# Kernel optimization log

Measured on AMD Instinct MI355X. Metric: run time of the kernel, lower is better.

The kernel has to match this reference:

```python
import jax, jax.numpy as jnp
import numpy as np

N_NODES = 100000
N_EDGES = 100000
D = 256
N_SIDE = 2  # rel_list = [side_a, side_b, rel_c, rel_d]
N_REL = 2


def setup_inputs() -> dict:
    key = jax.random.key(0)
    ks = jax.random.split(key, 7)
    h = jax.random.normal(ks[0], (N_NODES, D), dtype=jnp.float32)
    src_idx = jax.random.randint(ks[1], (N_SIDE + N_REL, N_EDGES), 0, N_NODES)
    dst_idx = jax.random.randint(ks[2], (N_SIDE + N_REL, N_EDGES), 0, N_NODES)
    # shared bilinear matrix R (nn.Linear(D, D, bias=False): y = x @ R_W.T)
    R_W = jax.random.normal(ks[3], (D, D), dtype=jnp.float32) * (1.0 / np.sqrt(D))
    # per-'side*' diagonal parameters (xavier over [D,1] then squeeze)
    d_side = jax.random.normal(ks[4], (N_SIDE, D), dtype=jnp.float32)
    # per-regular-relation Linear weights (with bias)
    W_rel = jax.random.normal(ks[5], (N_REL, D, D), dtype=jnp.float32) * (1.0 / np.sqrt(D))
    b_rel = jax.random.normal(ks[6], (N_REL, D), dtype=jnp.float32) * 0.01
    return {"h": h, "src_idx": src_idx, "dst_idx": dst_idx,
            "R_W": R_W, "d_side": d_side, "W_rel": W_rel, "b_rel": b_rel}


def reference(h, src_idx, dst_idx, R_W, d_side, W_rel, b_rel):
    # --- 'side*' edge types: score = (((h_u * d) @ R_W.T) * d) . h_v ---
    hu_s = h[src_idx[:N_SIDE]]            # [S, E, D] gather
    hv_s = h[dst_idx[:N_SIDE]]            # [S, E, D]
    lft = hu_s * d_side[:, None, :]       # [S, E, D]
    lft = jnp.einsum('sed,fd->sef', lft, R_W)  # Linear, no bias
    lft = lft * d_side[:, None, :]
    score_side = jnp.einsum('sed,sed->se', lft, hv_s)  # [S, E]

    # --- regular edge types: score = (h_u @ W.T + b) . h_v ---
    hu_r = h[src_idx[N_SIDE:]]            # [R, E, D]
    hv_r = h[dst_idx[N_SIDE:]]            # [R, E, D]
    lft_r = jnp.einsum('red,rfd->ref', hu_r, W_rel) + b_rel[:, None, :]
    score_rel = jnp.einsum('red,red->re', lft_r, hv_r)  # [R, E]

    return jnp.concatenate([score_side, score_rel], axis=0)  # [S+R, E]
```

## Files before the change

kernel.cpp:

```cpp
#include <hip/hip_runtime.h>
#include <stdint.h>

#define NNODES 100000
#define NEDGES 100000
#define DIM    256
#define NCH    4
#define ET     64
#define NT     1563
#define NBX    64
#define RSF    264
#define CONVB  2048
#define ZEROB  391

typedef _Float16 f16x8 __attribute__((ext_vector_type(8)));
typedef _Float16 f16x4 __attribute__((ext_vector_type(4)));
typedef float f32x4  __attribute__((ext_vector_type(4)));

__global__ void prep_fused(const float* __restrict__ RW,
                           const float* __restrict__ dside,
                           const float* __restrict__ Wrel,
                           const float* __restrict__ h,
                           _Float16* __restrict__ Bh, _Float16* __restrict__ Bl,
                           _Float16* __restrict__ H16,
                           float* __restrict__ out) {
    if (blockIdx.x < 128) {
        int t = blockIdx.x * blockDim.x + threadIdx.x;
        int lane = t & 63;
        int ft   = (t >> 6) & 15;
        int kc   = (t >> 10) & 7;
        int c    = t >> 13;
        int quad = lane >> 4, col = lane & 15;
        int f     = ft * 16 + col;
        int kbase = kc * 32 + quad * 8;

        f16x8 vh, vl;
#pragma unroll
        for (int j = 0; j < 8; ++j) {
            int k = kbase + j;
            float val;
            if (c < 2) {
                val = dside[c * DIM + f] * RW[f * DIM + k] * dside[c * DIM + k];
            } else {
                val = Wrel[(size_t)(c - 2) * DIM * DIM + f * DIM + k];
            }
            _Float16 hi = (_Float16)val;
            vh[j] = hi;
            vl[j] = (_Float16)(val - (float)hi);
        }
        ((f16x8*)Bh)[t] = vh;
        ((f16x8*)Bl)[t] = vl;
    } else if (blockIdx.x < 128 + ZEROB) {
        int i4 = (blockIdx.x - 128) * 256 + (int)threadIdx.x;
        if (i4 < NCH * NEDGES / 4)
            ((f32x4*)out)[i4] = (f32x4){0.f, 0.f, 0.f, 0.f};
    } else {
        const int total4 = NNODES * DIM / 4;
        const int stride = CONVB * 256;
        int i = (blockIdx.x - 128 - ZEROB) * 256 + (int)threadIdx.x;
        const f32x4* s4 = (const f32x4*)h;
        f16x4* d4 = (f16x4*)H16;
        for (; i + stride < total4; i += 2 * stride) {
            f32x4 a = s4[i];
            f32x4 b = s4[i + stride];
            f16x4 oa, ob;
#pragma unroll
            for (int j = 0; j < 4; ++j) { oa[j] = (_Float16)a[j]; ob[j] = (_Float16)b[j]; }
            d4[i] = oa; d4[i + stride] = ob;
        }
        if (i < total4) {
            f32x4 a = s4[i];
            f16x4 o;
#pragma unroll
            for (int j = 0; j < 4; ++j) o[j] = (_Float16)a[j];
            d4[i] = o;
        }
    }
}

__device__ __forceinline__ float dpp_reduce16(float s) {
    union { float f; int i; } u, v;
    u.f = s; v.i = __builtin_amdgcn_update_dpp(0, u.i, 0xB1,  0xF, 0xF, true); s += v.f;
    u.f = s; v.i = __builtin_amdgcn_update_dpp(0, u.i, 0x4E,  0xF, 0xF, true); s += v.f;
    u.f = s; v.i = __builtin_amdgcn_update_dpp(0, u.i, 0x141, 0xF, 0xF, true); s += v.f;
    u.f = s; v.i = __builtin_amdgcn_update_dpp(0, u.i, 0x140, 0xF, 0xF, true); s += v.f;
    return s;
}

__global__ __launch_bounds__(512, 1)
void edge_kernel(const _Float16* __restrict__ H16,
                 const int* __restrict__ src_idx,
                 const int* __restrict__ dst_idx,
                 const float* __restrict__ brel,
                 const _Float16* __restrict__ Bh_sw,
                 const _Float16* __restrict__ Bl_sw,
                 float* __restrict__ out) {
    const int c    = blockIdx.y;
    const int tid  = threadIdx.x;
    const int w    = tid >> 6;
    const int lane = tid & 63;
    const int quad = lane >> 4, col = lane & 15;

    __shared__ __align__(16) _Float16 s_a0[ET * RSF];
    __shared__ __align__(16) _Float16 s_v0[ET * RSF];
    __shared__ __align__(16) _Float16 s_a1[ET * RSF];
    __shared__ __align__(16) _Float16 s_v1[ET * RSF];

    f16x8 Bh_r[8][2], Bl_r[8][2];
    {
        const f16x8* bh = (const f16x8*)Bh_sw;
        const f16x8* bl = (const f16x8*)Bl_sw;
#pragma unroll
        for (int kc = 0; kc < 8; ++kc)
#pragma unroll
            for (int ftl = 0; ftl < 2; ++ftl) {
                int o = ((c * 8 + kc) * 16 + (w * 2 + ftl)) * 64 + lane;
                Bh_r[kc][ftl] = bh[o];
                Bl_r[kc][ftl] = bl[o];
            }
    }
#pragma unroll
    for (int kc = 0; kc < 8; ++kc)
#pragma unroll
        for (int ftl = 0; ftl < 2; ++ftl)
            asm volatile("" : "+v"(Bh_r[kc][ftl]), "+v"(Bl_r[kc][ftl]));

    float bias[2];
#pragma unroll
    for (int ftl = 0; ftl < 2; ++ftl) {
        int f = (w * 2 + ftl) * 16 + col;
        bias[ftl] = (c >= 2) ? brel[(size_t)(c - 2) * DIM + f] : 0.f;
    }

    const int  j8   = lane & 7;
    const bool isV  = (lane & 8) != 0;
    const int* ibase = (isV ? dst_idx : src_idx) + (size_t)c * NEDGES;

    auto loadpack = [&](int t) -> int {
        int e = t * ET + w * 8 + j8;
        if (e >= NEDGES) e = NEDGES - 1;
        return ibase[e];
    };

    const int t0 = blockIdx.x;
    f16x4 pA[8], pV[8];
    {
        int ip = loadpack(t0);
#pragma unroll
        for (int i = 0; i < 8; ++i) {
            int ia = __builtin_amdgcn_readlane(ip, i);
            int iv = __builtin_amdgcn_readlane(ip, 8 + i);
            pA[i] = *(const f16x4*)(H16 + (size_t)ia * DIM + lane * 4);
            pV[i] = *(const f16x4*)(H16 + (size_t)iv * DIM + lane * 4);
        }
    }
    int ipk0 = 0, ipk1 = 0;
    if (t0 + NBX < NT) ipk1 = loadpack(t0 + NBX);

    auto body = [&](int t, _Float16* sa, _Float16* sv, int& ipkUse, int& ipkLoad) {
#pragma unroll
        for (int i = 0; i < 8; ++i) {
            int lr = w * 8 + i;
            *(f16x4*)&sa[lr * RSF + lane * 4] = pA[i];
            *(f16x4*)&sv[lr * RSF + lane * 4] = pV[i];
        }

        if (t + 2 * NBX < NT) ipkLoad = loadpack(t + 2 * NBX);
        if (t + NBX < NT) {
#pragma unroll
            for (int i = 0; i < 8; ++i) {
                int ia = __builtin_amdgcn_readlane(ipkUse, i);
                int iv = __builtin_amdgcn_readlane(ipkUse, 8 + i);
                pA[i] = *(const f16x4*)(H16 + (size_t)ia * DIM + lane * 4);
                pV[i] = *(const f16x4*)(H16 + (size_t)iv * DIM + lane * 4);
            }
        }

        __syncthreads();

        f32x4 acc[4][2];
#pragma unroll
        for (int mt = 0; mt < 4; ++mt)
#pragma unroll
            for (int ftl = 0; ftl < 2; ++ftl) acc[mt][ftl] = (f32x4){0.f, 0.f, 0.f, 0.f};

#pragma unroll
        for (int kc = 0; kc < 8; ++kc) {
            f16x8 A[4];
#pragma unroll
            for (int mt = 0; mt < 4; ++mt)
                A[mt] = *(const f16x8*)&sa[(mt * 16 + col) * RSF + kc * 32 + quad * 8];
#pragma unroll
            for (int ftl = 0; ftl < 2; ++ftl) {
#pragma unroll
                for (int mt = 0; mt < 4; ++mt)
                    acc[mt][ftl] = __builtin_amdgcn_mfma_f32_16x16x32_f16(A[mt], Bh_r[kc][ftl], acc[mt][ftl], 0, 0, 0);
#pragma unroll
                for (int mt = 0; mt < 4; ++mt)
                    acc[mt][ftl] = __builtin_amdgcn_mfma_f32_16x16x32_f16(A[mt], Bl_r[kc][ftl], acc[mt][ftl], 0, 0, 0);
            }
        }

#pragma unroll
        for (int mt = 0; mt < 4; ++mt) {
            float ps[4];
#pragma unroll
            for (int r = 0; r < 4; ++r) {
                int el = mt * 16 + quad * 4 + r;
                float s = 0.f;
#pragma unroll
                for (int ftl = 0; ftl < 2; ++ftl) {
                    int f = (w * 2 + ftl) * 16 + col;
                    float v = (float)sv[el * RSF + f];
                    s += (acc[mt][ftl][r] + bias[ftl]) * v;
                }
                ps[r] = dpp_reduce16(s);
            }
            if (col == 0) {
#pragma unroll
                for (int r = 0; r < 4; ++r) {
                    int e = t * ET + mt * 16 + quad * 4 + r;
                    if (e < NEDGES)
                        atomicAdd(&out[(size_t)c * NEDGES + e], ps[r]);
                }
            }
        }
    };

    int t = t0;
    while (true) {
        body(t, s_a0, s_v0, ipk1, ipk0);
        t += NBX; if (t >= NT) break;
        body(t, s_a1, s_v1, ipk0, ipk1);
        t += NBX; if (t >= NT) break;
    }
}

extern "C" void kernel_launch(void* const* d_in, const int* in_sizes, int n_in,
                              void* d_out, int out_size, void* d_ws, size_t ws_size,
                              hipStream_t stream) {
    const float* hmat  = (const float*)d_in[0];
    const int*   src   = (const int*)d_in[1];
    const int*   dst   = (const int*)d_in[2];
    const float* RW    = (const float*)d_in[3];
    const float* dside = (const float*)d_in[4];
    const float* Wrel  = (const float*)d_in[5];
    const float* brel  = (const float*)d_in[6];
    float* out = (float*)d_out;

    const size_t nB = (size_t)NCH * DIM * DIM;
    _Float16* Bh  = (_Float16*)d_ws;
    _Float16* Bl  = Bh + nB;
    _Float16* H16 = Bl + nB;

    prep_fused<<<dim3(128 + ZEROB + CONVB), dim3(256), 0, stream>>>(
        RW, dside, Wrel, hmat, Bh, Bl, H16, out);

    dim3 grid(NBX, NCH);
    edge_kernel<<<grid, dim3(512), 0, stream>>>(H16, src, dst, brel, Bh, Bl, out);
}
```

Measured before the change: 290.3 us.

## Replace per-edge global atomics with LDS cross-wave reduction and direct stores

Each wave now writes its per-edge partial scores into a double-buffered shared array. The previous tile's eight partials are summed by 64 threads after the next tile's barrier, and the result is written with a plain store. This removes the global atomicAdd traffic and the separate zero-fill of the output in the prep kernel. In exchange it adds a small LDS buffer and a final barrier-and-reduce step after the loop.

```diff
diff --git a/kernel.cpp b/kernel.cpp
--- a/kernel.cpp
+++ b/kernel.cpp
@@ -10,7 +10,6 @@
 #define NBX    64
 #define RSF    264
 #define CONVB  2048
-#define ZEROB  391
 
 typedef _Float16 f16x8 __attribute__((ext_vector_type(8)));
 typedef _Float16 f16x4 __attribute__((ext_vector_type(4)));
@@ -21,8 +20,7 @@
                            const float* __restrict__ Wrel,
                            const float* __restrict__ h,
                            _Float16* __restrict__ Bh, _Float16* __restrict__ Bl,
-                           _Float16* __restrict__ H16,
-                           float* __restrict__ out) {
+                           _Float16* __restrict__ H16) {
     if (blockIdx.x < 128) {
         int t = blockIdx.x * blockDim.x + threadIdx.x;
         int lane = t & 63;
@@ -49,14 +47,10 @@
         }
         ((f16x8*)Bh)[t] = vh;
         ((f16x8*)Bl)[t] = vl;
-    } else if (blockIdx.x < 128 + ZEROB) {
-        int i4 = (blockIdx.x - 128) * 256 + (int)threadIdx.x;
-        if (i4 < NCH * NEDGES / 4)
-            ((f32x4*)out)[i4] = (f32x4){0.f, 0.f, 0.f, 0.f};
     } else {
         const int total4 = NNODES * DIM / 4;
         const int stride = CONVB * 256;
-        int i = (blockIdx.x - 128 - ZEROB) * 256 + (int)threadIdx.x;
+        int i = (blockIdx.x - 128) * 256 + (int)threadIdx.x;
         const f32x4* s4 = (const f32x4*)h;
         f16x4* d4 = (f16x4*)H16;
         for (; i + stride < total4; i += 2 * stride) {
@@ -104,6 +98,7 @@
     __shared__ __align__(16) _Float16 s_v0[ET * RSF];
     __shared__ __align__(16) _Float16 s_a1[ET * RSF];
     __shared__ __align__(16) _Float16 s_v1[ET * RSF];
+    __shared__ float red[2][8][ET];
 
     f16x8 Bh_r[8][2], Bl_r[8][2];
     {
@@ -156,7 +151,9 @@
     int ipk0 = 0, ipk1 = 0;
     if (t0 + NBX < NT) ipk1 = loadpack(t0 + NBX);
 
-    auto body = [&](int t, _Float16* sa, _Float16* sv, int& ipkUse, int& ipkLoad) {
+    auto body = [&](int t, int tPrev, _Float16* sa, _Float16* sv,
+                    float (*redW)[ET], float (*redR)[ET],
+                    int& ipkUse, int& ipkLoad) {
 #pragma unroll
         for (int i = 0; i < 8; ++i) {
             int lr = w * 8 + i;
@@ -176,6 +173,16 @@
         }
 
         __syncthreads();
+
+        if (tPrev >= 0 && tid < ET) {
+            int e = tPrev * ET + tid;
+            if (e < NEDGES) {
+                float s = 0.f;
+#pragma unroll
+                for (int i = 0; i < 8; ++i) s += redR[i][tid];
+                out[(size_t)c * NEDGES + e] = s;
+            }
+        }
 
         f32x4 acc[4][2];
 #pragma unroll
@@ -217,21 +224,30 @@
             }
             if (col == 0) {
 #pragma unroll
-                for (int r = 0; r < 4; ++r) {
-                    int e = t * ET + mt * 16 + quad * 4 + r;
-                    if (e < NEDGES)
-                        atomicAdd(&out[(size_t)c * NEDGES + e], ps[r]);
-                }
+                for (int r = 0; r < 4; ++r)
+                    redW[w][mt * 16 + quad * 4 + r] = ps[r];
             }
         }
     };
 
-    int t = t0;
+    int t = t0, prev = -1, par = 0;
     while (true) {
-        body(t, s_a0, s_v0, ipk1, ipk0);
-        t += NBX; if (t >= NT) break;
-        body(t, s_a1, s_v1, ipk0, ipk1);
-        t += NBX; if (t >= NT) break;
+        if (par == 0) body(t, prev, s_a0, s_v0, red[0], red[1], ipk1, ipk0);
+        else          body(t, prev, s_a1, s_v1, red[1], red[0], ipk0, ipk1);
+        prev = t; t += NBX;
+        if (t >= NT) break;
+        par ^= 1;
+    }
+
+    __syncthreads();
+    if (tid < ET) {
+        int e = prev * ET + tid;
+        if (e < NEDGES) {
+            float s = 0.f;
+#pragma unroll
+            for (int i = 0; i < 8; ++i) s += red[par][i][tid];
+            out[(size_t)c * NEDGES + e] = s;
+        }
     }
 }
 
@@ -252,8 +268,8 @@
     _Float16* Bl  = Bh + nB;
     _Float16* H16 = Bl + nB;
 
-    prep_fused<<<dim3(128 + ZEROB + CONVB), dim3(256), 0, stream>>>(
-        RW, dside, Wrel, hmat, Bh, Bl, H16, out);
+    prep_fused<<<dim3(128 + CONVB), dim3(256), 0, stream>>>(
+        RW, dside, Wrel, hmat, Bh, Bl, H16);
 
     dim3 grid(NBX, NCH);
     edge_kernel<<<grid, dim3(512), 0, stream>>>(H16, src, dst, brel, Bh, Bl, out);
```

Result: slower. 323.4 us (+11.4%).
